# Performance work log

Measured on AMD Instinct MI355X. Metric: run time of the kernel, lower is better.

Reference implementation:

```python
import jax, jax.numpy as jnp
import numpy as np

# Module hyperparameters (from init_kwargs / config defaults)
LOCAL_WINDOW = 128
GLOBAL_BUDGET = 64
ATT_BUDGET = 0.05
RANDOM_BUDGET = 0.1

B, S, D = 4, 4096, 1024


def setup_inputs() -> dict:
    key = jax.random.key(0)
    k1, k2 = jax.random.split(key)
    return {
        "hidden_states": jax.random.normal(k1, (B, S, D), dtype=jnp.float32),
        "attention_mask": jnp.ones((B, S), dtype=jnp.int32),
        "W_imp": jax.random.normal(k2, (1, D), dtype=jnp.float32) * 0.02,
    }


def _build_sparse_mask(hidden_states, attention_mask, W_imp):
    b, s, d = hidden_states.shape
    valid = attention_mask.astype(bool)                       # [b, s]
    # base mask: valid x valid, with causal constraint (is_decoder=True)
    i = jnp.arange(s)[:, None]
    j = jnp.arange(s)[None, :]
    causal = j <= i                                            # [s, s]
    base = (valid[:, None, :] & valid[:, :, None]) & causal[None]

    # 1) local causal sliding window: query i attends keys in [i-W+1, i]
    diff = i - j
    local = (diff >= 0) & (diff < LOCAL_WINDOW)                # [s, s]
    sparse = jnp.broadcast_to(local[None], (b, s, s))
    selected = jnp.broadcast_to(local.any(axis=0)[None], (b, s))

    # 2) global tokens via importance projection + top-k
    base_budget = min(GLOBAL_BUDGET, max(1, int(s * ATT_BUDGET)))
    scores = jnp.einsum('bsd,d->bs', hidden_states, W_imp[0])  # [b, s]
    scores = jnp.where(valid, scores, -jnp.inf)
    _, top_idx = jax.lax.top_k(scores, base_budget)            # [b, k]
    global_tokens = jnp.zeros((b, s), bool).at[
        jnp.arange(b)[:, None], top_idx].set(True)             # [b, s]
    # globals attend to everything and are attended by everything
    sparse = sparse | global_tokens[:, None, :] | global_tokens[:, :, None]
    selected = selected | global_tokens

    # 3) structured random tokens: deterministic strided selection
    r_budget = min(s, max(1, int(s * RANDOM_BUDGET)))
    stride = max(1, s // r_budget)
    rand_idx = (jnp.arange(r_budget) * stride) % s
    random_1d = jnp.zeros((s,), bool).at[rand_idx].set(True)
    random_tokens = jnp.broadcast_to(random_1d[None], (b, s))  # [b, s]
    sparse = sparse | random_tokens[:, None, :] | random_tokens[:, :, None]
    selected = selected | random_tokens

    # re-apply validity + causality
    sparse = sparse & base
    return sparse, selected, global_tokens, random_tokens


def reference(hidden_states, attention_mask, W_imp):
    b, s, _ = hidden_states.shape
    sparse, selected, gtok, rtok = _build_sparse_mask(
        hidden_states, attention_mask, W_imp)
    total_connections = sparse.sum(axis=(1, 2))
    attention_efficiency = total_connections.astype(jnp.float32) / float(s * s)
    # return sparse mask as float (the form consumed by attention), plus stats
    return (sparse.astype(jnp.float32), selected, attention_efficiency)
```

## Files before the change

kernel.cpp:

```cpp
#include <hip/hip_runtime.h>
#include <math.h>

#define BATCH 4
#define SEQ   4096
#define DIM   1024
#define TOPK  64
#define RSTRIDE 10
#define RBUDGET 409
#define LOCALW  128

typedef float nfloat4 __attribute__((ext_vector_type(4)));

#define WS_SCORES_OFF 0
#define WS_FLAGS_OFF  (BATCH * SEQ * sizeof(float))

#define X_TOPK_BLOCKS 4
#define X_SEL_BLOCKS  16
#define X_STATIC_BASE (X_TOPK_BLOCKS + X_SEL_BLOCKS)
#define Y_CNT_BLOCKS  4

__global__ void scores_kernel(const float* __restrict__ hs,
                              const int* __restrict__ amask,
                              const float* __restrict__ W,
                              float* __restrict__ scores) {
    int row  = blockIdx.x * 4 + (threadIdx.x >> 6);
    int lane = threadIdx.x & 63;
    const float4* h4 = (const float4*)(hs + (size_t)row * DIM);
    const float4* w4 = (const float4*)W;
    float acc = 0.0f;
#pragma unroll
    for (int k = 0; k < DIM / 4 / 64; ++k) {
        float4 h = h4[lane + 64 * k];
        float4 w = w4[lane + 64 * k];
        acc += h.x * w.x + h.y * w.y + h.z * w.z + h.w * w.w;
    }
#pragma unroll
    for (int off = 32; off; off >>= 1) acc += __shfl_down(acc, off, 64);
    if (lane == 0)
        scores[row] = amask[row] ? acc : -INFINITY;
}

__global__ void __launch_bounds__(256) fused_static_kernel(
        const float* __restrict__ scores,
        const int* __restrict__ amask,
        unsigned char* __restrict__ flags,
        float* __restrict__ out_sparse,
        float* __restrict__ out_selected) {
    __shared__ unsigned int su[SEQ];
    __shared__ unsigned char gsel[SEQ];
    __shared__ unsigned int hist[257];
    __shared__ unsigned int sufA[257];
    __shared__ unsigned int sufB[257];
    __shared__ unsigned int bcast[2];

    int bid = blockIdx.x;
    int t = threadIdx.x;

    if (bid < X_TOPK_BLOCKS) {
        int b = bid;

        for (int k = t; k < SEQ; k += 256) {
            float s = scores[b * SEQ + k];
            unsigned int x = __float_as_uint(s);
            su[k] = (x & 0x80000000u) ? ~x : (x | 0x80000000u);
            gsel[k] = 0;
        }
        __syncthreads();

        unsigned int prefixVal = 0;
        unsigned int remaining = TOPK;
#pragma unroll
        for (int pass = 0; pass < 4; ++pass) {
            int shift = 24 - 8 * pass;
            unsigned int highmask = (pass == 0) ? 0u : (0xFFFFFFFFu << (shift + 8));

            hist[t] = 0;
            if (t == 0) hist[256] = 0;
            __syncthreads();

#pragma unroll
            for (int e = 0; e < SEQ / 256; ++e) {
                unsigned int u = su[t * (SEQ / 256) + e];
                if ((u & highmask) == prefixVal)
                    atomicAdd(&hist[(u >> shift) & 0xFFu], 1u);
            }
            __syncthreads();

            sufA[t] = hist[t];
            if (t == 0) sufA[256] = 0;
            __syncthreads();
            unsigned int* src = sufA;
            unsigned int* dst = sufB;
            for (int d = 1; d < 256; d <<= 1) {
                unsigned int v = src[t] + ((t + d < 256) ? src[t + d] : 0u);
                dst[t] = v;
                if (t == 0) dst[256] = 0;
                __syncthreads();
                unsigned int* tmp = src; src = dst; dst = tmp;
            }
            if (src[t] >= remaining && src[t + 1] < remaining) {
                bcast[0] = (unsigned int)t;
                bcast[1] = remaining - src[t + 1];
            }
            __syncthreads();
            prefixVal |= (bcast[0] << shift);
            remaining = bcast[1];
            __syncthreads();
        }

        unsigned int T = prefixVal;
        unsigned int myeq = 0;
#pragma unroll
        for (int e = 0; e < SEQ / 256; ++e)
            if (su[t * (SEQ / 256) + e] == T) myeq++;
        sufA[t] = myeq;
        __syncthreads();
        {
            unsigned int* src = sufA;
            unsigned int* dst = sufB;
            for (int d = 1; d < 256; d <<= 1) {
                unsigned int v = src[t] + ((t >= d) ? src[t - d] : 0u);
                dst[t] = v;
                __syncthreads();
                unsigned int* tmp = src; src = dst; dst = tmp;
            }
            unsigned int taken = src[t] - myeq;
#pragma unroll
            for (int e = 0; e < SEQ / 256; ++e) {
                int idx = t * (SEQ / 256) + e;
                unsigned int u = su[idx];
                if (u > T) gsel[idx] = 1;
                else if (u == T) { if (taken < remaining) gsel[idx] = 1; taken++; }
            }
        }
        __syncthreads();

        for (int k = t; k < SEQ; k += 256) {
            int valid = (amask[b * SEQ + k] != 0) ? 1 : 0;
            int g = gsel[k];
            int r = ((k % RSTRIDE) == 0 && (k / RSTRIDE) < RBUDGET) ? 1 : 0;
            flags[b * SEQ + k] = (unsigned char)(valid | (g << 1) | (r << 2));
        }
        return;
    }

    if (bid < X_STATIC_BASE) {
        int idx = (bid - X_TOPK_BLOCKS) * 256 + t;
        nfloat4 ones = {1.0f, 1.0f, 1.0f, 1.0f};
        __builtin_nontemporal_store(ones, ((nfloat4*)out_selected) + idx);
        return;
    }

    int row0 = (bid - X_STATIC_BASE) << 2;
    int b = row0 >> 12;

    const int4* am4 = (const int4*)(amask + b * SEQ);
    unsigned int validBits = 0;
#pragma unroll
    for (int k = 0; k < 4; ++k) {
        int4 m = am4[t + 256 * k];
        validBits |= (unsigned int)(m.x != 0) << (k * 4 + 0);
        validBits |= (unsigned int)(m.y != 0) << (k * 4 + 1);
        validBits |= (unsigned int)(m.z != 0) << (k * 4 + 2);
        validBits |= (unsigned int)(m.w != 0) << (k * 4 + 3);
    }
    int4 mr = *(const int4*)(amask + row0);
    int vIr[4] = {mr.x != 0, mr.y != 0, mr.z != 0, mr.w != 0};

#pragma unroll
    for (int r = 0; r < 4; ++r) {
        int i = (row0 + r) & (SEQ - 1);
        int vI = vIr[r];
        int c4 = (i <= 127) ? 0 : (((i - 127 + 15) & ~15) >> 2);
        nfloat4* outrow4 = (nfloat4*)(out_sparse + (size_t)(row0 + r) * SEQ);
#pragma unroll
        for (int k = 0; k < 4; ++k) {
            int j4 = t + 256 * k;
            if (j4 < c4) continue;
            int j0 = j4 << 2;
            nfloat4 v;
#pragma unroll
            for (int e = 0; e < 4; ++e) {
                int j = j0 + e;
                int one = (j <= i) & vI & (int)((validBits >> (k * 4 + e)) & 1u);
                v[e] = one ? 1.0f : 0.0f;
            }
            __builtin_nontemporal_store(v, outrow4 + j4);
        }
    }
}

__global__ void __launch_bounds__(256) fused_dynamic_kernel(
        const unsigned char* __restrict__ flags,
        float* __restrict__ out_sparse,
        float* __restrict__ out_eff) {
    __shared__ unsigned int vb[256], hb[256];
    __shared__ int tA[256], tB[256], tC[256], tD[256];
    __shared__ int exV[256], exH[256];
    __shared__ int red[256];

    int bid = blockIdx.x, t = threadIdx.x;

    if (bid < Y_CNT_BLOCKS) {
        int b = bid, base = b * SEQ;
        const unsigned char* fp = flags + base + t * 16;
        unsigned int myv = 0, myh = 0;
#pragma unroll
        for (int e = 0; e < 16; ++e) {
            unsigned char f = fp[e];
            unsigned int v = f & 1u;
            unsigned int h = v & ((f & 6u) ? 1u : 0u);
            myv |= v << e;
            myh |= h << e;
        }
        vb[t] = myv; hb[t] = myh;
        int sv = __popc(myv), sh = __popc(myh);
        tA[t] = sv; tC[t] = sh;
        __syncthreads();
        int* vsrc = tA; int* vdst = tB;
        int* hsrc = tC; int* hdst = tD;
        for (int d = 1; d < 256; d <<= 1) {
            int av = vsrc[t] + ((t >= d) ? vsrc[t - d] : 0);
            int ah = hsrc[t] + ((t >= d) ? hsrc[t - d] : 0);
            vdst[t] = av; hdst[t] = ah;
            __syncthreads();
            int* tmp = vsrc; vsrc = vdst; vdst = tmp;
            tmp = hsrc; hsrc = hdst; hdst = tmp;
        }
        exV[t] = vsrc[t] - sv;
        exH[t] = hsrc[t] - sh;
        __syncthreads();

        int exVt = exV[t];
        int exV8 = (t >= 8) ? exV[t - 8] : 0;
        int exH8 = (t >= 8) ? exH[t - 8] : 0;
        unsigned int vb8 = (t >= 8) ? vb[t - 8] : 0u;
        unsigned int hb8 = (t >= 8) ? hb[t - 8] : 0u;
        int cnt = 0;
#pragma unroll
        for (int e = 0; e < 16; ++e) {
            unsigned int m = (2u << e) - 1u;
            int validI = (int)((myv >> e) & 1u);
            int hotI   = (int)((myh >> e) & 1u);
            int cumVi = exVt + __popc(myv & m);
            int c;
            if (t >= 8) {
                int cumVm = exV8 + __popc(vb8 & m);
                int cumHm = exH8 + __popc(hb8 & m);
                c = hotI ? cumVi : (cumVi - cumVm + cumHm);
            } else {
                c = cumVi;
            }
            cnt += validI ? c : 0;
        }
        red[t] = cnt;
        __syncthreads();
        for (int s2 = 128; s2; s2 >>= 1) {
            if (t < s2) red[t] += red[t + s2];
            __syncthreads();
        }
        if (t == 0)
            out_eff[b] = (float)red[0] * (1.0f / ((float)SEQ * (float)SEQ));
        return;
    }

    int row0 = (bid - Y_CNT_BLOCKS) << 2;
    int b = row0 >> 12;

    const uchar4* f4 = (const uchar4*)(flags + b * SEQ);
    unsigned int validBits = 0, hotBits = 0;
#pragma unroll
    for (int k = 0; k < 4; ++k) {
        uchar4 f = f4[t + 256 * k];
        unsigned char fa[4] = {f.x, f.y, f.z, f.w};
#pragma unroll
        for (int e = 0; e < 4; ++e) {
            int idx = k * 4 + e;
            validBits |= (unsigned int)(fa[e] & 1u) << idx;
            hotBits   |= (unsigned int)((fa[e] & 6u) ? 1u : 0u) << idx;
        }
    }
    uchar4 fr = *(const uchar4*)(flags + row0);
    unsigned char fra[4] = {fr.x, fr.y, fr.z, fr.w};

#pragma unroll
    for (int r = 0; r < 4; ++r) {
        int i = (row0 + r) & (SEQ - 1);
        if (i <= 127) continue;
        int vI = fra[r] & 1;
        int hotI = (fra[r] & 6) != 0;
        int c4 = ((i - 127 + 15) & ~15) >> 2;
        nfloat4* outrow4 = (nfloat4*)(out_sparse + (size_t)(row0 + r) * SEQ);
#pragma unroll
        for (int k = 0; k < 4; ++k) {
            int j4 = t + 256 * k;
            if (j4 >= c4) continue;
            int j0 = j4 << 2;
            nfloat4 v;
#pragma unroll
            for (int e = 0; e < 4; ++e) {
                int idx = k * 4 + e;
                int j = j0 + e;
                int one = vI & (int)((validBits >> idx) & 1u)
                        & (((i - j) < LOCALW) | hotI | (int)((hotBits >> idx) & 1u));
                v[e] = one ? 1.0f : 0.0f;
            }
            __builtin_nontemporal_store(v, outrow4 + j4);
        }
    }
}

extern "C" void kernel_launch(void* const* d_in, const int* in_sizes, int n_in,
                              void* d_out, int out_size, void* d_ws, size_t ws_size,
                              hipStream_t stream) {
    const float* hs    = (const float*)d_in[0];
    const int*   amask = (const int*)d_in[1];
    const float* W     = (const float*)d_in[2];

    char* ws = (char*)d_ws;
    float*         scores = (float*)(ws + WS_SCORES_OFF);
    unsigned char* flags  = (unsigned char*)(ws + WS_FLAGS_OFF);

    float* out_sparse   = (float*)d_out;
    float* out_selected = out_sparse + (size_t)BATCH * SEQ * SEQ;
    float* out_eff      = out_selected + BATCH * SEQ;

    scores_kernel<<<BATCH * SEQ / 4, 256, 0, stream>>>(hs, amask, W, scores);
    fused_static_kernel<<<X_STATIC_BASE + BATCH * SEQ / 4, 256, 0, stream>>>(
        scores, amask, flags, out_sparse, out_selected);
    fused_dynamic_kernel<<<Y_CNT_BLOCKS + BATCH * SEQ / 4, 256, 0, stream>>>(
        flags, out_sparse, out_eff);
}
```

Before: 316.6 us.

## Fuse three kernels into one persistent cooperative kernel with grid syncs

Merges the scores, static mask and dynamic mask kernels into one cooperative persistent kernel of 1024 blocks, separated by grid-wide barriers. While most blocks write the static causal/valid mask, four blocks run top-k and then the efficiency count, so the serial top-k overlaps with the bulk output writes. This removes launch gaps and the idle tail where top-k ran alone. In exchange it adds grid.sync overhead and fixed block counts that may reduce memory-level parallelism. If the cooperative launch fails, it falls back to the old three launches.

```diff
diff --git a/kernel.cpp b/kernel.cpp
--- a/kernel.cpp
+++ b/kernel.cpp
@@ -1,5 +1,8 @@
 #include <hip/hip_runtime.h>
+#include <hip/hip_cooperative_groups.h>
 #include <math.h>
+
+namespace cg = cooperative_groups;
 
 #define BATCH 4
 #define SEQ   4096
@@ -9,22 +12,38 @@
 #define RBUDGET 409
 #define LOCALW  128
 
+#define TOTAL_ROWS   (BATCH * SEQ)
+#define TOTAL_GROUPS (TOTAL_ROWS / 4)
+
+#define GRID_BLKS   1024
+#define WRITER_BLKS 1020
+
 typedef float nfloat4 __attribute__((ext_vector_type(4)));
 
 #define WS_SCORES_OFF 0
 #define WS_FLAGS_OFF  (BATCH * SEQ * sizeof(float))
 
-#define X_TOPK_BLOCKS 4
-#define X_SEL_BLOCKS  16
-#define X_STATIC_BASE (X_TOPK_BLOCKS + X_SEL_BLOCKS)
-#define Y_CNT_BLOCKS  4
-
-__global__ void scores_kernel(const float* __restrict__ hs,
-                              const int* __restrict__ amask,
-                              const float* __restrict__ W,
-                              float* __restrict__ scores) {
-    int row  = blockIdx.x * 4 + (threadIdx.x >> 6);
-    int lane = threadIdx.x & 63;
+struct TkS {
+    unsigned int su[SEQ];
+    unsigned char gsel[SEQ];
+    unsigned int hist[257];
+    unsigned int sufA[257];
+    unsigned int sufB[257];
+    unsigned int bcast[2];
+};
+struct CntS {
+    unsigned int vb[256], hb[256];
+    int tA[256], tB[256], tC[256], tD[256];
+    int exV[256], exH[256];
+    int red[256];
+};
+union SMemU { TkS tk; CntS cnt; };
+
+__device__ __forceinline__ void score_row(const float* __restrict__ hs,
+                                          const int* __restrict__ amask,
+                                          const float* __restrict__ W,
+                                          float* __restrict__ scores,
+                                          int row, int lane) {
     const float4* h4 = (const float4*)(hs + (size_t)row * DIM);
     const float4* w4 = (const float4*)W;
     float acc = 0.0f;
@@ -40,120 +59,162 @@
         scores[row] = amask[row] ? acc : -INFINITY;
 }
 
-__global__ void __launch_bounds__(256) fused_static_kernel(
-        const float* __restrict__ scores,
-        const int* __restrict__ amask,
-        unsigned char* __restrict__ flags,
-        float* __restrict__ out_sparse,
-        float* __restrict__ out_selected) {
-    __shared__ unsigned int su[SEQ];
-    __shared__ unsigned char gsel[SEQ];
-    __shared__ unsigned int hist[257];
-    __shared__ unsigned int sufA[257];
-    __shared__ unsigned int sufB[257];
-    __shared__ unsigned int bcast[2];
-
-    int bid = blockIdx.x;
-    int t = threadIdx.x;
-
-    if (bid < X_TOPK_BLOCKS) {
-        int b = bid;
-
-        for (int k = t; k < SEQ; k += 256) {
-            float s = scores[b * SEQ + k];
-            unsigned int x = __float_as_uint(s);
-            su[k] = (x & 0x80000000u) ? ~x : (x | 0x80000000u);
-            gsel[k] = 0;
-        }
-        __syncthreads();
-
-        unsigned int prefixVal = 0;
-        unsigned int remaining = TOPK;
-#pragma unroll
-        for (int pass = 0; pass < 4; ++pass) {
-            int shift = 24 - 8 * pass;
-            unsigned int highmask = (pass == 0) ? 0u : (0xFFFFFFFFu << (shift + 8));
-
-            hist[t] = 0;
-            if (t == 0) hist[256] = 0;
+__device__ void topk_body(const float* __restrict__ scores,
+                          const int* __restrict__ amask,
+                          unsigned char* __restrict__ flags,
+                          int b, int t, TkS& s) {
+    for (int k = t; k < SEQ; k += 256) {
+        float sc = scores[b * SEQ + k];
+        unsigned int x = __float_as_uint(sc);
+        s.su[k] = (x & 0x80000000u) ? ~x : (x | 0x80000000u);
+        s.gsel[k] = 0;
+    }
+    __syncthreads();
+
+    unsigned int prefixVal = 0;
+    unsigned int remaining = TOPK;
+#pragma unroll
+    for (int pass = 0; pass < 4; ++pass) {
+        int shift = 24 - 8 * pass;
+        unsigned int highmask = (pass == 0) ? 0u : (0xFFFFFFFFu << (shift + 8));
+
+        s.hist[t] = 0;
+        if (t == 0) s.hist[256] = 0;
+        __syncthreads();
+
+#pragma unroll
+        for (int e = 0; e < SEQ / 256; ++e) {
+            unsigned int u = s.su[t * (SEQ / 256) + e];
+            if ((u & highmask) == prefixVal)
+                atomicAdd(&s.hist[(u >> shift) & 0xFFu], 1u);
+        }
+        __syncthreads();
+
+        s.sufA[t] = s.hist[t];
+        if (t == 0) s.sufA[256] = 0;
+        __syncthreads();
+        unsigned int* src = s.sufA;
+        unsigned int* dst = s.sufB;
+        for (int d = 1; d < 256; d <<= 1) {
+            unsigned int v = src[t] + ((t + d < 256) ? src[t + d] : 0u);
+            dst[t] = v;
+            if (t == 0) dst[256] = 0;
             __syncthreads();
-
-#pragma unroll
-            for (int e = 0; e < SEQ / 256; ++e) {
-                unsigned int u = su[t * (SEQ / 256) + e];
-                if ((u & highmask) == prefixVal)
-                    atomicAdd(&hist[(u >> shift) & 0xFFu], 1u);
-            }
+            unsigned int* tmp = src; src = dst; dst = tmp;
+        }
+        if (src[t] >= remaining && src[t + 1] < remaining) {
+            s.bcast[0] = (unsigned int)t;
+            s.bcast[1] = remaining - src[t + 1];
+        }
+        __syncthreads();
+        prefixVal |= (s.bcast[0] << shift);
+        remaining = s.bcast[1];
+        __syncthreads();
+    }
+
+    unsigned int T = prefixVal;
+    unsigned int myeq = 0;
+#pragma unroll
+    for (int e = 0; e < SEQ / 256; ++e)
+        if (s.su[t * (SEQ / 256) + e] == T) myeq++;
+    s.sufA[t] = myeq;
+    __syncthreads();
+    {
+        unsigned int* src = s.sufA;
+        unsigned int* dst = s.sufB;
+        for (int d = 1; d < 256; d <<= 1) {
+            unsigned int v = src[t] + ((t >= d) ? src[t - d] : 0u);
+            dst[t] = v;
             __syncthreads();
-
-            sufA[t] = hist[t];
-            if (t == 0) sufA[256] = 0;
-            __syncthreads();
-            unsigned int* src = sufA;
-            unsigned int* dst = sufB;
-            for (int d = 1; d < 256; d <<= 1) {
-                unsigned int v = src[t] + ((t + d < 256) ? src[t + d] : 0u);
-                dst[t] = v;
-                if (t == 0) dst[256] = 0;
-                __syncthreads();
-                unsigned int* tmp = src; src = dst; dst = tmp;
-            }
-            if (src[t] >= remaining && src[t + 1] < remaining) {
-                bcast[0] = (unsigned int)t;
-                bcast[1] = remaining - src[t + 1];
-            }
-            __syncthreads();
-            prefixVal |= (bcast[0] << shift);
-            remaining = bcast[1];
-            __syncthreads();
-        }
-
-        unsigned int T = prefixVal;
-        unsigned int myeq = 0;
-#pragma unroll
-        for (int e = 0; e < SEQ / 256; ++e)
-            if (su[t * (SEQ / 256) + e] == T) myeq++;
-        sufA[t] = myeq;
-        __syncthreads();
-        {
-            unsigned int* src = sufA;
-            unsigned int* dst = sufB;
-            for (int d = 1; d < 256; d <<= 1) {
-                unsigned int v = src[t] + ((t >= d) ? src[t - d] : 0u);
-                dst[t] = v;
-                __syncthreads();
-                unsigned int* tmp = src; src = dst; dst = tmp;
-            }
-            unsigned int taken = src[t] - myeq;
-#pragma unroll
-            for (int e = 0; e < SEQ / 256; ++e) {
-                int idx = t * (SEQ / 256) + e;
-                unsigned int u = su[idx];
-                if (u > T) gsel[idx] = 1;
-                else if (u == T) { if (taken < remaining) gsel[idx] = 1; taken++; }
-            }
-        }
-        __syncthreads();
-
-        for (int k = t; k < SEQ; k += 256) {
-            int valid = (amask[b * SEQ + k] != 0) ? 1 : 0;
-            int g = gsel[k];
-            int r = ((k % RSTRIDE) == 0 && (k / RSTRIDE) < RBUDGET) ? 1 : 0;
-            flags[b * SEQ + k] = (unsigned char)(valid | (g << 1) | (r << 2));
-        }
-        return;
-    }
-
-    if (bid < X_STATIC_BASE) {
-        int idx = (bid - X_TOPK_BLOCKS) * 256 + t;
-        nfloat4 ones = {1.0f, 1.0f, 1.0f, 1.0f};
-        __builtin_nontemporal_store(ones, ((nfloat4*)out_selected) + idx);
-        return;
-    }
-
-    int row0 = (bid - X_STATIC_BASE) << 2;
+            unsigned int* tmp = src; src = dst; dst = tmp;
+        }
+        unsigned int taken = src[t] - myeq;
+#pragma unroll
+        for (int e = 0; e < SEQ / 256; ++e) {
+            int idx = t * (SEQ / 256) + e;
+            unsigned int u = s.su[idx];
+            if (u > T) s.gsel[idx] = 1;
+            else if (u == T) { if (taken < remaining) s.gsel[idx] = 1; taken++; }
+        }
+    }
+    __syncthreads();
+
+    for (int k = t; k < SEQ; k += 256) {
+        int valid = (amask[b * SEQ + k] != 0) ? 1 : 0;
+        int g = s.gsel[k];
+        int r = ((k % RSTRIDE) == 0 && (k / RSTRIDE) < RBUDGET) ? 1 : 0;
+        flags[b * SEQ + k] = (unsigned char)(valid | (g << 1) | (r << 2));
+    }
+}
+
+__device__ void counts_body(const unsigned char* __restrict__ flags,
+                            float* __restrict__ out_eff,
+                            int b, int t, CntS& s) {
+    int base = b * SEQ;
+    const unsigned char* fp = flags + base + t * 16;
+    unsigned int myv = 0, myh = 0;
+#pragma unroll
+    for (int e = 0; e < 16; ++e) {
+        unsigned char f = fp[e];
+        unsigned int v = f & 1u;
+        unsigned int h = v & ((f & 6u) ? 1u : 0u);
+        myv |= v << e;
+        myh |= h << e;
+    }
+    s.vb[t] = myv; s.hb[t] = myh;
+    int sv = __popc(myv), sh = __popc(myh);
+    s.tA[t] = sv; s.tC[t] = sh;
+    __syncthreads();
+    int* vsrc = s.tA; int* vdst = s.tB;
+    int* hsrc = s.tC; int* hdst = s.tD;
+    for (int d = 1; d < 256; d <<= 1) {
+        int av = vsrc[t] + ((t >= d) ? vsrc[t - d] : 0);
+        int ah = hsrc[t] + ((t >= d) ? hsrc[t - d] : 0);
+        vdst[t] = av; hdst[t] = ah;
+        __syncthreads();
+        int* tmp = vsrc; vsrc = vdst; vdst = tmp;
+        tmp = hsrc; hsrc = hdst; hdst = tmp;
+    }
+    s.exV[t] = vsrc[t] - sv;
+    s.exH[t] = hsrc[t] - sh;
+    __syncthreads();
+
+    int exVt = s.exV[t];
+    int exV8 = (t >= 8) ? s.exV[t - 8] : 0;
+    int exH8 = (t >= 8) ? s.exH[t - 8] : 0;
+    unsigned int vb8 = (t >= 8) ? s.vb[t - 8] : 0u;
+    unsigned int hb8 = (t >= 8) ? s.hb[t - 8] : 0u;
+    int cnt = 0;
+#pragma unroll
+    for (int e = 0; e < 16; ++e) {
+        unsigned int m = (2u << e) - 1u;
+        int validI = (int)((myv >> e) & 1u);
+        int hotI   = (int)((myh >> e) & 1u);
+        int cumVi = exVt + __popc(myv & m);
+        int c;
+        if (t >= 8) {
+            int cumVm = exV8 + __popc(vb8 & m);
+            int cumHm = exH8 + __popc(hb8 & m);
+            c = hotI ? cumVi : (cumVi - cumVm + cumHm);
+        } else {
+            c = cumVi;
+        }
+        cnt += validI ? c : 0;
+    }
+    s.red[t] = cnt;
+    __syncthreads();
+    for (int s2 = 128; s2; s2 >>= 1) {
+        if (t < s2) s.red[t] += s.red[t + s2];
+        __syncthreads();
+    }
+    if (t == 0)
+        out_eff[b] = (float)s.red[0] * (1.0f / ((float)SEQ * (float)SEQ));
+}
+
+__device__ __forceinline__ void static4(const int* __restrict__ amask,
+                                        float* __restrict__ out,
+                                        int row0, int t) {
     int b = row0 >> 12;
-
     const int4* am4 = (const int4*)(amask + b * SEQ);
     unsigned int validBits = 0;
 #pragma unroll
@@ -172,7 +233,7 @@
         int i = (row0 + r) & (SEQ - 1);
         int vI = vIr[r];
         int c4 = (i <= 127) ? 0 : (((i - 127 + 15) & ~15) >> 2);
-        nfloat4* outrow4 = (nfloat4*)(out_sparse + (size_t)(row0 + r) * SEQ);
+        nfloat4* outrow4 = (nfloat4*)(out + (size_t)(row0 + r) * SEQ);
 #pragma unroll
         for (int k = 0; k < 4; ++k) {
             int j4 = t + 256 * k;
@@ -190,83 +251,10 @@
     }
 }
 
-__global__ void __launch_bounds__(256) fused_dynamic_kernel(
-        const unsigned char* __restrict__ flags,
-        float* __restrict__ out_sparse,
-        float* __restrict__ out_eff) {
-    __shared__ unsigned int vb[256], hb[256];
-    __shared__ int tA[256], tB[256], tC[256], tD[256];
-    __shared__ int exV[256], exH[256];
-    __shared__ int red[256];
-
-    int bid = blockIdx.x, t = threadIdx.x;
-
-    if (bid < Y_CNT_BLOCKS) {
-        int b = bid, base = b * SEQ;
-        const unsigned char* fp = flags + base + t * 16;
-        unsigned int myv = 0, myh = 0;
-#pragma unroll
-        for (int e = 0; e < 16; ++e) {
-            unsigned char f = fp[e];
-            unsigned int v = f & 1u;
-            unsigned int h = v & ((f & 6u) ? 1u : 0u);
-            myv |= v << e;
-            myh |= h << e;
-        }
-        vb[t] = myv; hb[t] = myh;
-        int sv = __popc(myv), sh = __popc(myh);
-        tA[t] = sv; tC[t] = sh;
-        __syncthreads();
-        int* vsrc = tA; int* vdst = tB;
-        int* hsrc = tC; int* hdst = tD;
-        for (int d = 1; d < 256; d <<= 1) {
-            int av = vsrc[t] + ((t >= d) ? vsrc[t - d] : 0);
-            int ah = hsrc[t] + ((t >= d) ? hsrc[t - d] : 0);
-            vdst[t] = av; hdst[t] = ah;
-            __syncthreads();
-            int* tmp = vsrc; vsrc = vdst; vdst = tmp;
-            tmp = hsrc; hsrc = hdst; hdst = tmp;
-        }
-        exV[t] = vsrc[t] - sv;
-        exH[t] = hsrc[t] - sh;
-        __syncthreads();
-
-        int exVt = exV[t];
-        int exV8 = (t >= 8) ? exV[t - 8] : 0;
-        int exH8 = (t >= 8) ? exH[t - 8] : 0;
-        unsigned int vb8 = (t >= 8) ? vb[t - 8] : 0u;
-        unsigned int hb8 = (t >= 8) ? hb[t - 8] : 0u;
-        int cnt = 0;
-#pragma unroll
-        for (int e = 0; e < 16; ++e) {
-            unsigned int m = (2u << e) - 1u;
-            int validI = (int)((myv >> e) & 1u);
-            int hotI   = (int)((myh >> e) & 1u);
-            int cumVi = exVt + __popc(myv & m);
-            int c;
-            if (t >= 8) {
-                int cumVm = exV8 + __popc(vb8 & m);
-                int cumHm = exH8 + __popc(hb8 & m);
-                c = hotI ? cumVi : (cumVi - cumVm + cumHm);
-            } else {
-                c = cumVi;
-            }
-            cnt += validI ? c : 0;
-        }
-        red[t] = cnt;
-        __syncthreads();
-        for (int s2 = 128; s2; s2 >>= 1) {
-            if (t < s2) red[t] += red[t + s2];
-            __syncthreads();
-        }
-        if (t == 0)
-            out_eff[b] = (float)red[0] * (1.0f / ((float)SEQ * (float)SEQ));
-        return;
-    }
-
-    int row0 = (bid - Y_CNT_BLOCKS) << 2;
+__device__ __forceinline__ void dynamic4(const unsigned char* __restrict__ flags,
+                                         float* __restrict__ out,
+                                         int row0, int t) {
     int b = row0 >> 12;
-
     const uchar4* f4 = (const uchar4*)(flags + b * SEQ);
     unsigned int validBits = 0, hotBits = 0;
 #pragma unroll
@@ -290,7 +278,7 @@
         int vI = fra[r] & 1;
         int hotI = (fra[r] & 6) != 0;
         int c4 = ((i - 127 + 15) & ~15) >> 2;
-        nfloat4* outrow4 = (nfloat4*)(out_sparse + (size_t)(row0 + r) * SEQ);
+        nfloat4* outrow4 = (nfloat4*)(out + (size_t)(row0 + r) * SEQ);
 #pragma unroll
         for (int k = 0; k < 4; ++k) {
             int j4 = t + 256 * k;
@@ -310,6 +298,92 @@
     }
 }
 
+__global__ void __launch_bounds__(256, 4) fused_all(
+        const float* __restrict__ hs,
+        const int* __restrict__ amask,
+        const float* __restrict__ W,
+        float* __restrict__ scores,
+        unsigned char* __restrict__ flags,
+        float* __restrict__ out_sparse,
+        float* __restrict__ out_selected,
+        float* __restrict__ out_eff) {
+    __shared__ SMemU sm;
+    cg::grid_group grid = cg::this_grid();
+    int bid = blockIdx.x, t = threadIdx.x;
+
+    {
+        int wid = bid * 4 + (t >> 6);
+        int lane = t & 63;
+#pragma unroll
+        for (int rr = 0; rr < 4; ++rr)
+            score_row(hs, amask, W, scores, wid + 4096 * rr, lane);
+    }
+    __threadfence();
+    grid.sync();
+
+    if (bid >= WRITER_BLKS) {
+        int b = bid - WRITER_BLKS;
+        topk_body(scores, amask, flags, b, t, sm.tk);
+        __syncthreads();
+        counts_body(flags, out_eff, b, t, sm.cnt);
+    } else {
+        if (bid < 16) {
+            nfloat4 ones = {1.0f, 1.0f, 1.0f, 1.0f};
+            __builtin_nontemporal_store(ones,
+                ((nfloat4*)out_selected) + bid * 256 + t);
+        }
+        for (int g = bid; g < TOTAL_GROUPS; g += WRITER_BLKS)
+            static4(amask, out_sparse, g << 2, t);
+    }
+    __threadfence();
+    grid.sync();
+
+    for (int g = bid; g < TOTAL_GROUPS; g += GRID_BLKS)
+        dynamic4(flags, out_sparse, g << 2, t);
+}
+
+__global__ void scores_kernel(const float* __restrict__ hs,
+                              const int* __restrict__ amask,
+                              const float* __restrict__ W,
+                              float* __restrict__ scores) {
+    int row  = blockIdx.x * 4 + (threadIdx.x >> 6);
+    score_row(hs, amask, W, scores, row, threadIdx.x & 63);
+}
+
+__global__ void __launch_bounds__(256) fused_static_kernel(
+        const float* __restrict__ scores,
+        const int* __restrict__ amask,
+        unsigned char* __restrict__ flags,
+        float* __restrict__ out_sparse,
+        float* __restrict__ out_selected) {
+    __shared__ TkS tks;
+    int bid = blockIdx.x, t = threadIdx.x;
+    if (bid < BATCH) {
+        topk_body(scores, amask, flags, bid, t, tks);
+        return;
+    }
+    if (bid < BATCH + 16) {
+        nfloat4 ones = {1.0f, 1.0f, 1.0f, 1.0f};
+        __builtin_nontemporal_store(ones,
+            ((nfloat4*)out_selected) + (bid - BATCH) * 256 + t);
+        return;
+    }
+    static4(amask, out_sparse, (bid - BATCH - 16) << 2, t);
+}
+
+__global__ void __launch_bounds__(256) fused_dynamic_kernel(
+        const unsigned char* __restrict__ flags,
+        float* __restrict__ out_sparse,
+        float* __restrict__ out_eff) {
+    __shared__ CntS cns;
+    int bid = blockIdx.x, t = threadIdx.x;
+    if (bid < BATCH) {
+        counts_body(flags, out_eff, bid, t, cns);
+        return;
+    }
+    dynamic4(flags, out_sparse, (bid - BATCH) << 2, t);
+}
+
 extern "C" void kernel_launch(void* const* d_in, const int* in_sizes, int n_in,
                               void* d_out, int out_size, void* d_ws, size_t ws_size,
                               hipStream_t stream) {
@@ -325,9 +399,16 @@
     float* out_selected = out_sparse + (size_t)BATCH * SEQ * SEQ;
     float* out_eff      = out_selected + BATCH * SEQ;
 
-    scores_kernel<<<BATCH * SEQ / 4, 256, 0, stream>>>(hs, amask, W, scores);
-    fused_static_kernel<<<X_STATIC_BASE + BATCH * SEQ / 4, 256, 0, stream>>>(
-        scores, amask, flags, out_sparse, out_selected);
-    fused_dynamic_kernel<<<Y_CNT_BLOCKS + BATCH * SEQ / 4, 256, 0, stream>>>(
-        flags, out_sparse, out_eff);
-}
+    void* args[] = {(void*)&hs, (void*)&amask, (void*)&W, (void*)&scores,
+                    (void*)&flags, (void*)&out_sparse, (void*)&out_selected,
+                    (void*)&out_eff};
+    hipError_t e = hipLaunchCooperativeKernel(fused_all, dim3(GRID_BLKS),
+                                              dim3(256), args, 0u, stream);
+    if (e != hipSuccess) {
+        scores_kernel<<<TOTAL_ROWS / 4, 256, 0, stream>>>(hs, amask, W, scores);
+        fused_static_kernel<<<BATCH + 16 + TOTAL_GROUPS, 256, 0, stream>>>(
+            scores, amask, flags, out_sparse, out_selected);
+        fused_dynamic_kernel<<<BATCH + TOTAL_GROUPS, 256, 0, stream>>>(
+            flags, out_sparse, out_eff);
+    }
+}
```

New measurement: 722.1 us. 2.28x slower.
